# Performance work log

Measured on AMD Instinct MI355X. Metric: run time of the kernel, lower is better.

Reference implementation:

```python
import jax, jax.numpy as jnp
import numpy as np

B, N, D, H = 256, 64, 128, 64

def _w(key, shape, fan_in):
    return jax.random.normal(key, shape, jnp.float32) * (1.0 / np.sqrt(fan_in))

def setup_inputs() -> dict:
    key = jax.random.key(0)
    ks = jax.random.split(key, 6)
    return {
        "observations": jax.random.normal(ks[0], (B, N, D), jnp.float32),
        "enc_w": _w(ks[1], (D, H), D), "enc_b": jnp.zeros((H,), jnp.float32),
        "gate_w1": _w(ks[2], (2 * H, H), 2 * H), "gate_b1": jnp.zeros((H,), jnp.float32),
        "gate_w2": _w(ks[3], (H, 1), H), "gate_b2": jnp.zeros((1,), jnp.float32),
        "msg_w1": _w(ks[4], (H, H), H), "msg_b1": jnp.zeros((H,), jnp.float32),
        "msg_w2": _w(ks[5], (H, H), H), "msg_b2": jnp.zeros((H,), jnp.float32),
    }

def reference(observations, enc_w, enc_b, gate_w1, gate_b1, gate_w2, gate_b2,
              msg_w1, msg_b1, msg_w2, msg_b2):
    # encoder: (B, N, H)
    enc = jax.nn.relu(observations @ enc_w + enc_b)
    h = enc.shape[-1]
    # gate layer 1 on concat([e_i, e_j]) == e_i @ W_top + e_j @ W_bot; avoids
    # materializing the (B, N, N, 2H) concat tensor.
    w_i, w_j = gate_w1[:h], gate_w1[h:]
    gi = enc @ w_i                       # (B, N, H) contribution of receiver i
    gj = enc @ w_j + gate_b1             # (B, N, H) contribution of sender j
    hid = jax.nn.relu(gi[:, :, None, :] + gj[:, None, :, :])   # (B, N, N, H)
    gates = jax.nn.sigmoid(jnp.squeeze(hid @ gate_w2, -1) + gate_b2[0])  # (B, N, N)
    # message_gen(encoded): identical for every i in the original loop
    msg = jax.nn.relu(enc @ msg_w1 + msg_b1) @ msg_w2 + msg_b2  # (B, N, H)
    # enhanced[b, i] = sum_j gates[b, i, j] * msg[b, j]
    enhanced = jnp.einsum('bij,bjh->bih', gates, msg)           # (B, N, H)
    return enhanced
```

## Files before the change

### kernel.cpp

```cpp
#include <hip/hip_runtime.h>

typedef float  f32x4  __attribute__((ext_vector_type(4)));
typedef short  bf16x8 __attribute__((ext_vector_type(8)));

#define Bb 256

__device__ __forceinline__ uint cvtpk(float lo, float hi) {
    uint r;
    asm("v_cvt_pk_bf16_f32 %0, %1, %2" : "=v"(r) : "v"(lo), "v"(hi));
    return r;
}
__device__ __forceinline__ ushort f2b1(float v) { return (ushort)cvtpk(v, v); }
__device__ __forceinline__ float bflo(uint u) { return __uint_as_float(u << 16); }
__device__ __forceinline__ float bfhi(uint u) { return __uint_as_float(u & 0xffff0000u); }

union U8 { uint u[4]; bf16x8 v; };

__global__ __launch_bounds__(512, 4) void gcm_kernel(
    const float* __restrict__ obs,
    const float* __restrict__ enc_w,
    const float* __restrict__ enc_b,
    const float* __restrict__ gate_w1,
    const float* __restrict__ gate_b1,
    const float* __restrict__ gate_w2,
    const float* __restrict__ gate_b2,
    const float* __restrict__ msg_w1,
    const float* __restrict__ msg_b1,
    const float* __restrict__ msg_w2,
    const float* __restrict__ msg_b2,
    float* __restrict__ out)
{
    const int bid  = blockIdx.x;
    const int bb   = bid >> 1;
    const int half = bid & 1;
    const int t    = threadIdx.x;
    const int lane = t & 63;
    const int wv   = t >> 6;
    const int lr   = lane & 15;
    const int lg   = lane >> 4;
    const int rt   = wv >> 1;

    __shared__ __align__(16) char arena[74240];
    ushort* s_wT     = (ushort*)(arena);
    ushort* s_encwT  = (ushort*)(arena + 32768);
    float*  s_gi     = (float*) (arena + 32768);
    ushort* s_gatesb = (ushort*)(arena + 40960);
    ushort* s_enc    = (ushort*)(arena + 49152);
    ushort* s_msgT   = (ushort*)(arena + 49152);
    ushort* s_msgh   = (ushort*)(arena + 57344);
    ushort* s_gjb    = (ushort*)(arena + 65536);

    float4 pf[8];
    {
        const float* ob = obs + ((size_t)bb * 64 + rt * 16 + lr) * 128 + lg * 8;
        #pragma unroll
        for (int ks = 0; ks < 4; ++ks) {
            pf[2 * ks]     = *(const float4*)(ob + ks * 32);
            pf[2 * ks + 1] = *(const float4*)(ob + ks * 32 + 4);
        }
    }
    float4 pe[4];
    #pragma unroll
    for (int it = 0; it < 4; ++it) {
        const int idx = t + it * 512;
        const int k   = idx >> 4;
        const int n0  = (idx & 15) * 4;
        pe[it] = *(const float4*)(enc_w + k * 64 + n0);
    }
    bf16x8 afrag[4];
    #pragma unroll
    for (int ks = 0; ks < 4; ++ks) {
        U8 u;
        u.u[0] = cvtpk(pf[2 * ks].x,     pf[2 * ks].y);
        u.u[1] = cvtpk(pf[2 * ks].z,     pf[2 * ks].w);
        u.u[2] = cvtpk(pf[2 * ks + 1].x, pf[2 * ks + 1].y);
        u.u[3] = cvtpk(pf[2 * ks + 1].z, pf[2 * ks + 1].w);
        afrag[ks] = u.v;
    }
    #pragma unroll
    for (int it = 0; it < 4; ++it) {
        const int idx = t + it * 512;
        const int k   = idx >> 4;
        const int n0  = (idx & 15) * 4;
        uint pA = cvtpk(pe[it].x, pe[it].y), pB = cvtpk(pe[it].z, pe[it].w);
        s_encwT[((n0 + 0) * 128 + k) ^ (((n0 + 0) & 7) << 3)] = (ushort)pA;
        s_encwT[((n0 + 1) * 128 + k) ^ (((n0 + 1) & 7) << 3)] = (ushort)(pA >> 16);
        s_encwT[((n0 + 2) * 128 + k) ^ (((n0 + 2) & 7) << 3)] = (ushort)pB;
        s_encwT[((n0 + 3) * 128 + k) ^ (((n0 + 3) & 7) << 3)] = (ushort)(pB >> 16);
    }
    float4 pfw[8];
    {
        const int k  = t >> 4;
        const int n0 = (t & 15) * 4;
        #pragma unroll
        for (int kh = 0; kh < 2; ++kh) {
            const int kk = k + kh * 32;
            pfw[0 * 2 + kh] = *(const float4*)(gate_w1 + kk * 64 + n0);
            pfw[1 * 2 + kh] = *(const float4*)(gate_w1 + (64 + kk) * 64 + n0);
            pfw[2 * 2 + kh] = *(const float4*)(msg_w1 + kk * 64 + n0);
            pfw[3 * 2 + kh] = *(const float4*)(msg_w2 + kk * 64 + n0);
        }
    }
    __syncthreads();

    {
        f32x4 acc[2];
        acc[0] = (f32x4){0.f, 0.f, 0.f, 0.f};
        acc[1] = (f32x4){0.f, 0.f, 0.f, 0.f};
        #pragma unroll
        for (int ks = 0; ks < 4; ++ks) {
            const int k0 = ks * 32 + lg * 8;
            #pragma unroll
            for (int jj = 0; jj < 2; ++jj) {
                const int n = (wv & 1) * 32 + jj * 16 + lr;
                bf16x8 bf = *(const bf16x8*)(s_encwT + ((n * 128 + k0) ^ ((n & 7) << 3)));
                acc[jj] = __builtin_amdgcn_mfma_f32_16x16x32_bf16(afrag[ks], bf, acc[jj], 0, 0, 0);
            }
        }
        {
            const int k  = t >> 4;
            const int n00 = (t & 15) * 4;
            #pragma unroll
            for (int m = 0; m < 4; ++m) {
                #pragma unroll
                for (int kh = 0; kh < 2; ++kh) {
                    float4 w4 = pfw[m * 2 + kh];
                    const int kk = k + kh * 32;
                    const int nb = m * 64 + n00;
                    uint pA = cvtpk(w4.x, w4.y), pB = cvtpk(w4.z, w4.w);
                    s_wT[((nb + 0) * 64 + kk) ^ (((nb + 0) & 7) << 3)] = (ushort)pA;
                    s_wT[((nb + 1) * 64 + kk) ^ (((nb + 1) & 7) << 3)] = (ushort)(pA >> 16);
                    s_wT[((nb + 2) * 64 + kk) ^ (((nb + 2) & 7) << 3)] = (ushort)pB;
                    s_wT[((nb + 3) * 64 + kk) ^ (((nb + 3) & 7) << 3)] = (ushort)(pB >> 16);
                }
            }
        }
        const int rb = rt * 16 + lg * 4;
        #pragma unroll
        for (int jj = 0; jj < 2; ++jj) {
            const int n = (wv & 1) * 32 + jj * 16 + lr;
            const float be = enc_b[n];
            #pragma unroll
            for (int rr = 0; rr < 4; ++rr) {
                const int row = rb + rr;
                float v = fmaxf(acc[jj][rr] + be, 0.f);
                s_enc[(row * 64 + n) ^ ((row & 7) << 3)] = f2b1(v);
            }
        }
    }
    __syncthreads();

    {
        f32x4 acc[6];
        #pragma unroll
        for (int q = 0; q < 6; ++q) acc[q] = (f32x4){0.f, 0.f, 0.f, 0.f};
        const int arow = rt * 16 + lr;
        #pragma unroll
        for (int ks = 0; ks < 2; ++ks) {
            const int k0 = ks * 32 + lg * 8;
            bf16x8 a = *(const bf16x8*)(s_enc + ((arow * 64 + k0) ^ ((arow & 7) << 3)));
            #pragma unroll
            for (int q = 0; q < 6; ++q) {
                const int n = ((wv & 1) * 6 + q) * 16 + lr;
                bf16x8 bf = *(const bf16x8*)(s_wT + ((n * 64 + k0) ^ ((n & 7) << 3)));
                acc[q] = __builtin_amdgcn_mfma_f32_16x16x32_bf16(a, bf, acc[q], 0, 0, 0);
            }
        }
        const int rb = rt * 16 + lg * 4;
        #pragma unroll
        for (int q = 0; q < 6; ++q) {
            const int nfull = ((wv & 1) * 6 + q) * 16;
            const int cc = nfull + lr;
            if (nfull < 64) {
                if ((rt >> 1) == half) {
                    const int lb = rb - half * 32;
                    #pragma unroll
                    for (int rr = 0; rr < 4; ++rr) {
                        const int row = lb + rr;
                        s_gi[(row * 64 + cc) ^ ((row & 7) << 2)] = acc[q][rr];
                    }
                }
            } else if (nfull < 128) {
                const float b1 = gate_b1[cc - 64];
                #pragma unroll
                for (int rr = 0; rr < 4; ++rr)
                    s_gjb[(rb + rr) * 68 + (cc - 64)] = f2b1(acc[q][rr] + b1);
            } else {
                const float bm = msg_b1[cc - 128];
                float v0 = fmaxf(acc[q][0] + bm, 0.f), v1 = fmaxf(acc[q][1] + bm, 0.f);
                float v2 = fmaxf(acc[q][2] + bm, 0.f), v3 = fmaxf(acc[q][3] + bm, 0.f);
                uint pA = cvtpk(v0, v1), pB = cvtpk(v2, v3);
                const int c2 = cc - 128;
                s_msgh[((rb + 0) * 64 + c2) ^ (((rb + 0) & 7) << 3)] = (ushort)pA;
                s_msgh[((rb + 1) * 64 + c2) ^ (((rb + 1) & 7) << 3)] = (ushort)(pA >> 16);
                s_msgh[((rb + 2) * 64 + c2) ^ (((rb + 2) & 7) << 3)] = (ushort)pB;
                s_msgh[((rb + 3) * 64 + c2) ^ (((rb + 3) & 7) << 3)] = (ushort)(pB >> 16);
            }
        }
    }
    __syncthreads();

    {
        f32x4 acc[2];
        acc[0] = (f32x4){0.f, 0.f, 0.f, 0.f};
        acc[1] = (f32x4){0.f, 0.f, 0.f, 0.f};
        const int arow = rt * 16 + lr;
        #pragma unroll
        for (int ks = 0; ks < 2; ++ks) {
            const int k0 = ks * 32 + lg * 8;
            bf16x8 a = *(const bf16x8*)(s_msgh + ((arow * 64 + k0) ^ ((arow & 7) << 3)));
            #pragma unroll
            for (int jj = 0; jj < 2; ++jj) {
                const int n = 192 + ((wv & 1) * 2 + jj) * 16 + lr;
                bf16x8 bf = *(const bf16x8*)(s_wT + ((n * 64 + k0) ^ ((n & 7) << 3)));
                acc[jj] = __builtin_amdgcn_mfma_f32_16x16x32_bf16(a, bf, acc[jj], 0, 0, 0);
            }
        }
        const int jb = rt * 16 + lg * 4;
        #pragma unroll
        for (int jj = 0; jj < 2; ++jj) {
            const int h = ((wv & 1) * 2 + jj) * 16 + lr;
            const float bm2 = msg_b2[h];
            uint pA = cvtpk(acc[jj][0] + bm2, acc[jj][1] + bm2);
            uint pB = cvtpk(acc[jj][2] + bm2, acc[jj][3] + bm2);
            const int e = (h * 64 + jb) ^ ((h & 7) << 3);
            *(uint*)(s_msgT + e)     = pA;
            *(uint*)(s_msgT + e + 2) = pB;
        }
    }

    {
        const int lrow0 = wv * 4;
        float ag[4] = {0.f, 0.f, 0.f, 0.f};
        const ushort* gjrow = s_gjb + lane * 68;
        #pragma unroll
        for (int h0 = 0; h0 < 64; h0 += 8) {
            uint2 pj0 = *(const uint2*)(gjrow + h0);
            uint2 pj1 = *(const uint2*)(gjrow + h0 + 4);
            float gj0 = bflo(pj0.x), gj1 = bfhi(pj0.x), gj2 = bflo(pj0.y), gj3 = bfhi(pj0.y);
            float gj4 = bflo(pj1.x), gj5 = bfhi(pj1.x), gj6 = bflo(pj1.y), gj7 = bfhi(pj1.y);
            float4 w2a = *(const float4*)(gate_w2 + h0);
            float4 w2b = *(const float4*)(gate_w2 + h0 + 4);
            #pragma unroll
            for (int r = 0; r < 4; ++r) {
                const int row = lrow0 + r;
                float4 gia = *(const float4*)(s_gi + ((row * 64 + h0) ^ ((row & 7) << 2)));
                float4 gib = *(const float4*)(s_gi + ((row * 64 + h0 + 4) ^ ((row & 7) << 2)));
                ag[r] = fmaf(fmaxf(gia.x + gj0, 0.f), w2a.x, ag[r]);
                ag[r] = fmaf(fmaxf(gia.y + gj1, 0.f), w2a.y, ag[r]);
                ag[r] = fmaf(fmaxf(gia.z + gj2, 0.f), w2a.z, ag[r]);
                ag[r] = fmaf(fmaxf(gia.w + gj3, 0.f), w2a.w, ag[r]);
                ag[r] = fmaf(fmaxf(gib.x + gj4, 0.f), w2b.x, ag[r]);
                ag[r] = fmaf(fmaxf(gib.y + gj5, 0.f), w2b.y, ag[r]);
                ag[r] = fmaf(fmaxf(gib.z + gj6, 0.f), w2b.z, ag[r]);
                ag[r] = fmaf(fmaxf(gib.w + gj7, 0.f), w2b.w, ag[r]);
            }
        }
        const float b2v = gate_b2[0];
        #pragma unroll
        for (int r = 0; r < 4; ++r) {
            const int row = lrow0 + r;
            const float g = 1.f / (1.f + __expf(-(ag[r] + b2v)));
            s_gatesb[(row * 64 + lane) ^ ((row & 7) << 3)] = f2b1(g);
        }
    }
    __syncthreads();

    {
        const int rtl = wv >> 2;
        const int ct  = wv & 3;
        f32x4 acc = (f32x4){0.f, 0.f, 0.f, 0.f};
        const int arow = rtl * 16 + lr;
        const int n = ct * 16 + lr;
        #pragma unroll
        for (int ks = 0; ks < 2; ++ks) {
            const int k0 = ks * 32 + lg * 8;
            bf16x8 a  = *(const bf16x8*)(s_gatesb + ((arow * 64 + k0) ^ ((arow & 7) << 3)));
            bf16x8 bf = *(const bf16x8*)(s_msgT   + ((n * 64 + k0) ^ ((n & 7) << 3)));
            acc = __builtin_amdgcn_mfma_f32_16x16x32_bf16(a, bf, acc, 0, 0, 0);
        }
        const int rb = half * 32 + rtl * 16 + lg * 4;
        #pragma unroll
        for (int rr = 0; rr < 4; ++rr)
            out[((size_t)bb * 64 + rb + rr) * 64 + n] = acc[rr];
    }
}

extern "C" void kernel_launch(void* const* d_in, const int* in_sizes, int n_in,
                              void* d_out, int out_size, void* d_ws, size_t ws_size,
                              hipStream_t stream) {
    const float* obs     = (const float*)d_in[0];
    const float* enc_w   = (const float*)d_in[1];
    const float* enc_b   = (const float*)d_in[2];
    const float* gate_w1 = (const float*)d_in[3];
    const float* gate_b1 = (const float*)d_in[4];
    const float* gate_w2 = (const float*)d_in[5];
    const float* gate_b2 = (const float*)d_in[6];
    const float* msg_w1  = (const float*)d_in[7];
    const float* msg_b1  = (const float*)d_in[8];
    const float* msg_w2  = (const float*)d_in[9];
    const float* msg_b2  = (const float*)d_in[10];
    float* out = (float*)d_out;

    gcm_kernel<<<2 * Bb, 512, 0, stream>>>(obs, enc_w, enc_b, gate_w1, gate_b1,
                                           gate_w2, gate_b2, msg_w1, msg_b1,
                                           msg_w2, msg_b2, out);
}
```

Measured before the change: 22.33 us.

## Split fused kernel into projection and gating kernels via workspace buffers

Splits the single fused kernel into two launches. The first computes encoder, gate projections and messages for only half the rows per block, removing the duplicated per-batch work, and writes gi, gj and transposed messages in bf16 to a global workspace. The second kernel computes the pairwise gates and the final einsum from those buffers. A single-kernel fallback with 1024 threads per block runs when the workspace is too small. The split adds an extra launch, a global round trip for the intermediates, and bf16 rounding of gi.

```diff
diff --git a/kernel.cpp b/kernel.cpp
--- a/kernel.cpp
+++ b/kernel.cpp
@@ -16,43 +16,34 @@
 
 union U8 { uint u[4]; bf16x8 v; };
 
-__global__ __launch_bounds__(512, 4) void gcm_kernel(
-    const float* __restrict__ obs,
-    const float* __restrict__ enc_w,
-    const float* __restrict__ enc_b,
-    const float* __restrict__ gate_w1,
-    const float* __restrict__ gate_b1,
-    const float* __restrict__ gate_w2,
-    const float* __restrict__ gate_b2,
-    const float* __restrict__ msg_w1,
-    const float* __restrict__ msg_b1,
-    const float* __restrict__ msg_w2,
+__global__ __launch_bounds__(512, 4) void gcm_ka(
+    const float* __restrict__ obs, const float* __restrict__ enc_w,
+    const float* __restrict__ enc_b, const float* __restrict__ gate_w1,
+    const float* __restrict__ gate_b1, const float* __restrict__ msg_w1,
+    const float* __restrict__ msg_b1, const float* __restrict__ msg_w2,
     const float* __restrict__ msg_b2,
-    float* __restrict__ out)
+    ushort* __restrict__ gi_g, ushort* __restrict__ gj_g, ushort* __restrict__ msgT_g)
 {
-    const int bid  = blockIdx.x;
-    const int bb   = bid >> 1;
-    const int half = bid & 1;
+    const int bid = blockIdx.x;
+    const int bb  = bid >> 1;
+    const int hR  = bid & 1;
     const int t    = threadIdx.x;
     const int lane = t & 63;
     const int wv   = t >> 6;
     const int lr   = lane & 15;
     const int lg   = lane >> 4;
-    const int rt   = wv >> 1;
-
-    __shared__ __align__(16) char arena[74240];
-    ushort* s_wT     = (ushort*)(arena);
-    ushort* s_encwT  = (ushort*)(arena + 32768);
-    float*  s_gi     = (float*) (arena + 32768);
-    ushort* s_gatesb = (ushort*)(arena + 40960);
-    ushort* s_enc    = (ushort*)(arena + 49152);
-    ushort* s_msgT   = (ushort*)(arena + 49152);
-    ushort* s_msgh   = (ushort*)(arena + 57344);
-    ushort* s_gjb    = (ushort*)(arena + 65536);
+    const int rt   = wv >> 2;
+    const int ct   = wv & 3;
+
+    __shared__ __align__(16) char arena[57344];
+    ushort* s_wT    = (ushort*)(arena);
+    ushort* s_encwT = (ushort*)(arena + 32768);
+    ushort* s_enc   = (ushort*)(arena + 49152);
+    ushort* s_msgh  = (ushort*)(arena + 53248);
 
     float4 pf[8];
     {
-        const float* ob = obs + ((size_t)bb * 64 + rt * 16 + lr) * 128 + lg * 8;
+        const float* ob = obs + ((size_t)bb * 64 + hR * 32 + rt * 16 + lr) * 128 + lg * 8;
         #pragma unroll
         for (int ks = 0; ks < 4; ++ks) {
             pf[2 * ks]     = *(const float4*)(ob + ks * 32);
@@ -104,21 +95,16 @@
     __syncthreads();
 
     {
-        f32x4 acc[2];
-        acc[0] = (f32x4){0.f, 0.f, 0.f, 0.f};
-        acc[1] = (f32x4){0.f, 0.f, 0.f, 0.f};
+        f32x4 acc = (f32x4){0.f, 0.f, 0.f, 0.f};
+        const int n = ct * 16 + lr;
         #pragma unroll
         for (int ks = 0; ks < 4; ++ks) {
             const int k0 = ks * 32 + lg * 8;
-            #pragma unroll
-            for (int jj = 0; jj < 2; ++jj) {
-                const int n = (wv & 1) * 32 + jj * 16 + lr;
-                bf16x8 bf = *(const bf16x8*)(s_encwT + ((n * 128 + k0) ^ ((n & 7) << 3)));
-                acc[jj] = __builtin_amdgcn_mfma_f32_16x16x32_bf16(afrag[ks], bf, acc[jj], 0, 0, 0);
-            }
+            bf16x8 bf = *(const bf16x8*)(s_encwT + ((n * 128 + k0) ^ ((n & 7) << 3)));
+            acc = __builtin_amdgcn_mfma_f32_16x16x32_bf16(afrag[ks], bf, acc, 0, 0, 0);
         }
         {
-            const int k  = t >> 4;
+            const int k   = t >> 4;
             const int n00 = (t & 15) * 4;
             #pragma unroll
             for (int m = 0; m < 4; ++m) {
@@ -136,55 +122,46 @@
             }
         }
         const int rb = rt * 16 + lg * 4;
-        #pragma unroll
-        for (int jj = 0; jj < 2; ++jj) {
-            const int n = (wv & 1) * 32 + jj * 16 + lr;
-            const float be = enc_b[n];
-            #pragma unroll
-            for (int rr = 0; rr < 4; ++rr) {
-                const int row = rb + rr;
-                float v = fmaxf(acc[jj][rr] + be, 0.f);
-                s_enc[(row * 64 + n) ^ ((row & 7) << 3)] = f2b1(v);
-            }
-        }
-    }
-    __syncthreads();
-
-    {
-        f32x4 acc[6];
-        #pragma unroll
-        for (int q = 0; q < 6; ++q) acc[q] = (f32x4){0.f, 0.f, 0.f, 0.f};
+        const float be = enc_b[n];
+        #pragma unroll
+        for (int rr = 0; rr < 4; ++rr) {
+            const int row = rb + rr;
+            float v = fmaxf(acc[rr] + be, 0.f);
+            s_enc[(row * 64 + n) ^ ((row & 7) << 3)] = f2b1(v);
+        }
+    }
+    __syncthreads();
+
+    {
+        f32x4 acc[3];
+        #pragma unroll
+        for (int q = 0; q < 3; ++q) acc[q] = (f32x4){0.f, 0.f, 0.f, 0.f};
         const int arow = rt * 16 + lr;
         #pragma unroll
         for (int ks = 0; ks < 2; ++ks) {
             const int k0 = ks * 32 + lg * 8;
             bf16x8 a = *(const bf16x8*)(s_enc + ((arow * 64 + k0) ^ ((arow & 7) << 3)));
             #pragma unroll
-            for (int q = 0; q < 6; ++q) {
-                const int n = ((wv & 1) * 6 + q) * 16 + lr;
+            for (int q = 0; q < 3; ++q) {
+                const int n = (ct * 3 + q) * 16 + lr;
                 bf16x8 bf = *(const bf16x8*)(s_wT + ((n * 64 + k0) ^ ((n & 7) << 3)));
                 acc[q] = __builtin_amdgcn_mfma_f32_16x16x32_bf16(a, bf, acc[q], 0, 0, 0);
             }
         }
         const int rb = rt * 16 + lg * 4;
         #pragma unroll
-        for (int q = 0; q < 6; ++q) {
-            const int nfull = ((wv & 1) * 6 + q) * 16;
+        for (int q = 0; q < 3; ++q) {
+            const int nfull = (ct * 3 + q) * 16;
             const int cc = nfull + lr;
             if (nfull < 64) {
-                if ((rt >> 1) == half) {
-                    const int lb = rb - half * 32;
-                    #pragma unroll
-                    for (int rr = 0; rr < 4; ++rr) {
-                        const int row = lb + rr;
-                        s_gi[(row * 64 + cc) ^ ((row & 7) << 2)] = acc[q][rr];
-                    }
-                }
+                #pragma unroll
+                for (int rr = 0; rr < 4; ++rr)
+                    gi_g[((size_t)bb * 64 + hR * 32 + rb + rr) * 64 + cc] = f2b1(acc[q][rr]);
             } else if (nfull < 128) {
                 const float b1 = gate_b1[cc - 64];
                 #pragma unroll
                 for (int rr = 0; rr < 4; ++rr)
-                    s_gjb[(rb + rr) * 68 + (cc - 64)] = f2b1(acc[q][rr] + b1);
+                    gj_g[((size_t)bb * 64 + hR * 32 + rb + rr) * 64 + (cc - 64)] = f2b1(acc[q][rr] + b1);
             } else {
                 const float bm = msg_b1[cc - 128];
                 float v0 = fmaxf(acc[q][0] + bm, 0.f), v1 = fmaxf(acc[q][1] + bm, 0.f);
@@ -201,77 +178,87 @@
     __syncthreads();
 
     {
-        f32x4 acc[2];
-        acc[0] = (f32x4){0.f, 0.f, 0.f, 0.f};
-        acc[1] = (f32x4){0.f, 0.f, 0.f, 0.f};
+        f32x4 acc = (f32x4){0.f, 0.f, 0.f, 0.f};
         const int arow = rt * 16 + lr;
+        const int n = 192 + ct * 16 + lr;
         #pragma unroll
         for (int ks = 0; ks < 2; ++ks) {
             const int k0 = ks * 32 + lg * 8;
-            bf16x8 a = *(const bf16x8*)(s_msgh + ((arow * 64 + k0) ^ ((arow & 7) << 3)));
-            #pragma unroll
-            for (int jj = 0; jj < 2; ++jj) {
-                const int n = 192 + ((wv & 1) * 2 + jj) * 16 + lr;
-                bf16x8 bf = *(const bf16x8*)(s_wT + ((n * 64 + k0) ^ ((n & 7) << 3)));
-                acc[jj] = __builtin_amdgcn_mfma_f32_16x16x32_bf16(a, bf, acc[jj], 0, 0, 0);
-            }
-        }
-        const int jb = rt * 16 + lg * 4;
-        #pragma unroll
-        for (int jj = 0; jj < 2; ++jj) {
-            const int h = ((wv & 1) * 2 + jj) * 16 + lr;
-            const float bm2 = msg_b2[h];
-            uint pA = cvtpk(acc[jj][0] + bm2, acc[jj][1] + bm2);
-            uint pB = cvtpk(acc[jj][2] + bm2, acc[jj][3] + bm2);
-            const int e = (h * 64 + jb) ^ ((h & 7) << 3);
-            *(uint*)(s_msgT + e)     = pA;
-            *(uint*)(s_msgT + e + 2) = pB;
-        }
-    }
-
-    {
-        const int lrow0 = wv * 4;
-        float ag[4] = {0.f, 0.f, 0.f, 0.f};
-        const ushort* gjrow = s_gjb + lane * 68;
-        #pragma unroll
-        for (int h0 = 0; h0 < 64; h0 += 8) {
-            uint2 pj0 = *(const uint2*)(gjrow + h0);
-            uint2 pj1 = *(const uint2*)(gjrow + h0 + 4);
-            float gj0 = bflo(pj0.x), gj1 = bfhi(pj0.x), gj2 = bflo(pj0.y), gj3 = bfhi(pj0.y);
-            float gj4 = bflo(pj1.x), gj5 = bfhi(pj1.x), gj6 = bflo(pj1.y), gj7 = bfhi(pj1.y);
-            float4 w2a = *(const float4*)(gate_w2 + h0);
-            float4 w2b = *(const float4*)(gate_w2 + h0 + 4);
-            #pragma unroll
-            for (int r = 0; r < 4; ++r) {
-                const int row = lrow0 + r;
-                float4 gia = *(const float4*)(s_gi + ((row * 64 + h0) ^ ((row & 7) << 2)));
-                float4 gib = *(const float4*)(s_gi + ((row * 64 + h0 + 4) ^ ((row & 7) << 2)));
-                ag[r] = fmaf(fmaxf(gia.x + gj0, 0.f), w2a.x, ag[r]);
-                ag[r] = fmaf(fmaxf(gia.y + gj1, 0.f), w2a.y, ag[r]);
-                ag[r] = fmaf(fmaxf(gia.z + gj2, 0.f), w2a.z, ag[r]);
-                ag[r] = fmaf(fmaxf(gia.w + gj3, 0.f), w2a.w, ag[r]);
-                ag[r] = fmaf(fmaxf(gib.x + gj4, 0.f), w2b.x, ag[r]);
-                ag[r] = fmaf(fmaxf(gib.y + gj5, 0.f), w2b.y, ag[r]);
-                ag[r] = fmaf(fmaxf(gib.z + gj6, 0.f), w2b.z, ag[r]);
-                ag[r] = fmaf(fmaxf(gib.w + gj7, 0.f), w2b.w, ag[r]);
-            }
-        }
-        const float b2v = gate_b2[0];
-        #pragma unroll
-        for (int r = 0; r < 4; ++r) {
-            const int row = lrow0 + r;
-            const float g = 1.f / (1.f + __expf(-(ag[r] + b2v)));
-            s_gatesb[(row * 64 + lane) ^ ((row & 7) << 3)] = f2b1(g);
-        }
-    }
-    __syncthreads();
-
-    {
-        const int rtl = wv >> 2;
-        const int ct  = wv & 3;
+            bf16x8 a  = *(const bf16x8*)(s_msgh + ((arow * 64 + k0) ^ ((arow & 7) << 3)));
+            bf16x8 bf = *(const bf16x8*)(s_wT + ((n * 64 + k0) ^ ((n & 7) << 3)));
+            acc = __builtin_amdgcn_mfma_f32_16x16x32_bf16(a, bf, acc, 0, 0, 0);
+        }
+        const int h  = ct * 16 + lr;
+        const int jg = hR * 32 + rt * 16 + lg * 4;
+        const float bm2 = msg_b2[h];
+        uint pA = cvtpk(acc[0] + bm2, acc[1] + bm2);
+        uint pB = cvtpk(acc[2] + bm2, acc[3] + bm2);
+        uint* dst = (uint*)(msgT_g + ((size_t)bb * 64 + h) * 64 + jg);
+        dst[0] = pA;
+        dst[1] = pB;
+    }
+}
+
+__global__ __launch_bounds__(512, 4) void gcm_kb(
+    const float* __restrict__ gate_w2, const float* __restrict__ gate_b2,
+    const ushort* __restrict__ gi_g, const ushort* __restrict__ gj_g,
+    const ushort* __restrict__ msgT_g, float* __restrict__ out)
+{
+    const int bid = blockIdx.x;
+    const int bb  = bid >> 1;
+    const int hR  = bid & 1;
+    const int t    = threadIdx.x;
+    const int lane = t & 63;
+    const int wv   = t >> 6;
+    const int lr   = lane & 15;
+    const int lg   = lane >> 4;
+
+    __shared__ __align__(16) ushort s_msgT[64 * 64];
+    __shared__ __align__(16) ushort s_gatesb[32 * 64];
+
+    {
+        const int h = t >> 3, q = t & 7;
+        uint4 v = *(const uint4*)(msgT_g + ((size_t)bb * 64 + h) * 64 + q * 8);
+        *(uint4*)(s_msgT + ((h * 64 + q * 8) ^ ((h & 7) << 3))) = v;
+    }
+
+    float gjv[64];
+    {
+        const ushort* gp = gj_g + ((size_t)bb * 64 + lane) * 64;
+        #pragma unroll
+        for (int c = 0; c < 8; ++c) {
+            uint4 p = *(const uint4*)(gp + c * 8);
+            gjv[c * 8 + 0] = bflo(p.x); gjv[c * 8 + 1] = bfhi(p.x);
+            gjv[c * 8 + 2] = bflo(p.y); gjv[c * 8 + 3] = bfhi(p.y);
+            gjv[c * 8 + 4] = bflo(p.z); gjv[c * 8 + 5] = bfhi(p.z);
+            gjv[c * 8 + 6] = bflo(p.w); gjv[c * 8 + 7] = bfhi(p.w);
+        }
+    }
+    const float b2v = gate_b2[0];
+
+    #pragma unroll
+    for (int r = 0; r < 4; ++r) {
+        const int lrow = wv * 4 + r;
+        const int grow = __builtin_amdgcn_readfirstlane(hR * 32 + lrow);
+        const uint* gip = (const uint*)(gi_g + ((size_t)bb * 64 + grow) * 64);
+        float acc = 0.f;
+        #pragma unroll
+        for (int c = 0; c < 32; ++c) {
+            const uint p = gip[c];
+            const float g0 = bflo(p), g1 = bfhi(p);
+            acc = fmaf(fmaxf(g0 + gjv[2 * c],     0.f), gate_w2[2 * c],     acc);
+            acc = fmaf(fmaxf(g1 + gjv[2 * c + 1], 0.f), gate_w2[2 * c + 1], acc);
+        }
+        const float g = 1.f / (1.f + __expf(-(acc + b2v)));
+        s_gatesb[(lrow * 64 + lane) ^ ((lrow & 7) << 3)] = f2b1(g);
+    }
+    __syncthreads();
+
+    {
+        const int rtl = wv >> 2, ctl = wv & 3;
         f32x4 acc = (f32x4){0.f, 0.f, 0.f, 0.f};
         const int arow = rtl * 16 + lr;
-        const int n = ct * 16 + lr;
+        const int n = ctl * 16 + lr;
         #pragma unroll
         for (int ks = 0; ks < 2; ++ks) {
             const int k0 = ks * 32 + lg * 8;
@@ -279,7 +266,220 @@
             bf16x8 bf = *(const bf16x8*)(s_msgT   + ((n * 64 + k0) ^ ((n & 7) << 3)));
             acc = __builtin_amdgcn_mfma_f32_16x16x32_bf16(a, bf, acc, 0, 0, 0);
         }
-        const int rb = half * 32 + rtl * 16 + lg * 4;
+        const int rb = hR * 32 + rtl * 16 + lg * 4;
+        #pragma unroll
+        for (int rr = 0; rr < 4; ++rr)
+            out[((size_t)bb * 64 + rb + rr) * 64 + n] = acc[rr];
+    }
+}
+
+__global__ __launch_bounds__(1024) void gcm_fb(
+    const float* __restrict__ obs, const float* __restrict__ enc_w,
+    const float* __restrict__ enc_b, const float* __restrict__ gate_w1,
+    const float* __restrict__ gate_b1, const float* __restrict__ gate_w2,
+    const float* __restrict__ gate_b2, const float* __restrict__ msg_w1,
+    const float* __restrict__ msg_b1, const float* __restrict__ msg_w2,
+    const float* __restrict__ msg_b2, float* __restrict__ out)
+{
+    const int bb   = blockIdx.x;
+    const int t    = threadIdx.x;
+    const int lane = t & 63;
+    const int wv   = t >> 6;
+    const int lr   = lane & 15;
+    const int lg   = lane >> 4;
+    const int rt   = wv & 3;
+    const int ct   = wv >> 2;
+
+    __shared__ __align__(16) ushort s_encwT[64 * 128];
+    __shared__ __align__(16) ushort s_wT[256 * 64];
+    __shared__ __align__(16) ushort s_enc[64 * 64];
+    __shared__ __align__(16) ushort s_msgh[64 * 64];
+    __shared__ __align__(16) ushort s_gatesb[64 * 64];
+    __shared__ __align__(16) ushort s_msgT[64 * 64];
+    __shared__ __align__(16) float  s_gi[64 * 64];
+    __shared__ __align__(16) float  s_gj[64 * 64];
+    __shared__ __align__(16) float  s_w2[64];
+
+    float4 pf[8];
+    {
+        const float* ob = obs + ((size_t)bb * 64 + rt * 16 + lr) * 128 + lg * 8;
+        #pragma unroll
+        for (int ks = 0; ks < 4; ++ks) {
+            pf[2 * ks]     = *(const float4*)(ob + ks * 32);
+            pf[2 * ks + 1] = *(const float4*)(ob + ks * 32 + 4);
+        }
+    }
+    if (t < 64) s_w2[t] = gate_w2[t];
+    #pragma unroll
+    for (int it = 0; it < 2; ++it) {
+        const int g  = t + it * 1024;
+        const int k  = g >> 4;
+        const int n0 = (g & 15) * 4;
+        float4 w4 = *(const float4*)(enc_w + k * 64 + n0);
+        uint pA = cvtpk(w4.x, w4.y), pB = cvtpk(w4.z, w4.w);
+        s_encwT[((n0 + 0) * 128 + k) ^ (((n0 + 0) & 7) << 3)] = (ushort)pA;
+        s_encwT[((n0 + 1) * 128 + k) ^ (((n0 + 1) & 7) << 3)] = (ushort)(pA >> 16);
+        s_encwT[((n0 + 2) * 128 + k) ^ (((n0 + 2) & 7) << 3)] = (ushort)pB;
+        s_encwT[((n0 + 3) * 128 + k) ^ (((n0 + 3) & 7) << 3)] = (ushort)(pB >> 16);
+    }
+    bf16x8 afrag[4];
+    #pragma unroll
+    for (int ks = 0; ks < 4; ++ks) {
+        U8 u;
+        u.u[0] = cvtpk(pf[2 * ks].x,     pf[2 * ks].y);
+        u.u[1] = cvtpk(pf[2 * ks].z,     pf[2 * ks].w);
+        u.u[2] = cvtpk(pf[2 * ks + 1].x, pf[2 * ks + 1].y);
+        u.u[3] = cvtpk(pf[2 * ks + 1].z, pf[2 * ks + 1].w);
+        afrag[ks] = u.v;
+    }
+    float4 pfw[4];
+    {
+        const int k  = t >> 4;
+        const int n0 = (t & 15) * 4;
+        pfw[0] = *(const float4*)(gate_w1 + k * 64 + n0);
+        pfw[1] = *(const float4*)(gate_w1 + (64 + k) * 64 + n0);
+        pfw[2] = *(const float4*)(msg_w1 + k * 64 + n0);
+        pfw[3] = *(const float4*)(msg_w2 + k * 64 + n0);
+    }
+    __syncthreads();
+    {
+        f32x4 acc = (f32x4){0.f, 0.f, 0.f, 0.f};
+        const int n = ct * 16 + lr;
+        #pragma unroll
+        for (int ks = 0; ks < 4; ++ks) {
+            const int k0 = ks * 32 + lg * 8;
+            bf16x8 bf = *(const bf16x8*)(s_encwT + ((n * 128 + k0) ^ ((n & 7) << 3)));
+            acc = __builtin_amdgcn_mfma_f32_16x16x32_bf16(afrag[ks], bf, acc, 0, 0, 0);
+        }
+        #pragma unroll
+        for (int it = 0; it < 4; ++it) {
+            const int k  = t >> 4;
+            const int n0 = it * 64 + (t & 15) * 4;
+            uint pA = cvtpk(pfw[it].x, pfw[it].y), pB = cvtpk(pfw[it].z, pfw[it].w);
+            s_wT[((n0 + 0) * 64 + k) ^ (((n0 + 0) & 7) << 3)] = (ushort)pA;
+            s_wT[((n0 + 1) * 64 + k) ^ (((n0 + 1) & 7) << 3)] = (ushort)(pA >> 16);
+            s_wT[((n0 + 2) * 64 + k) ^ (((n0 + 2) & 7) << 3)] = (ushort)pB;
+            s_wT[((n0 + 3) * 64 + k) ^ (((n0 + 3) & 7) << 3)] = (ushort)(pB >> 16);
+        }
+        const float be = enc_b[n];
+        float v0 = fmaxf(acc[0] + be, 0.f), v1 = fmaxf(acc[1] + be, 0.f);
+        float v2 = fmaxf(acc[2] + be, 0.f), v3 = fmaxf(acc[3] + be, 0.f);
+        uint pA = cvtpk(v0, v1), pB = cvtpk(v2, v3);
+        const int rb = rt * 16 + lg * 4;
+        s_enc[((rb + 0) * 64 + n) ^ (((rb + 0) & 7) << 3)] = (ushort)pA;
+        s_enc[((rb + 1) * 64 + n) ^ (((rb + 1) & 7) << 3)] = (ushort)(pA >> 16);
+        s_enc[((rb + 2) * 64 + n) ^ (((rb + 2) & 7) << 3)] = (ushort)pB;
+        s_enc[((rb + 3) * 64 + n) ^ (((rb + 3) & 7) << 3)] = (ushort)(pB >> 16);
+    }
+    __syncthreads();
+    {
+        f32x4 acc[3];
+        #pragma unroll
+        for (int q = 0; q < 3; ++q) acc[q] = (f32x4){0.f, 0.f, 0.f, 0.f};
+        const int arow = rt * 16 + lr;
+        #pragma unroll
+        for (int ks = 0; ks < 2; ++ks) {
+            const int k0 = ks * 32 + lg * 8;
+            bf16x8 a = *(const bf16x8*)(s_enc + ((arow * 64 + k0) ^ ((arow & 7) << 3)));
+            #pragma unroll
+            for (int q = 0; q < 3; ++q) {
+                const int n = (ct * 3 + q) * 16 + lr;
+                bf16x8 bf = *(const bf16x8*)(s_wT + ((n * 64 + k0) ^ ((n & 7) << 3)));
+                acc[q] = __builtin_amdgcn_mfma_f32_16x16x32_bf16(a, bf, acc[q], 0, 0, 0);
+            }
+        }
+        const int rb = rt * 16 + lg * 4;
+        #pragma unroll
+        for (int q = 0; q < 3; ++q) {
+            const int nfull = (ct * 3 + q) * 16;
+            const int cc = nfull + lr;
+            if (nfull < 64) {
+                #pragma unroll
+                for (int rr = 0; rr < 4; ++rr) {
+                    const int row = rb + rr;
+                    s_gi[(row * 64 + cc) ^ ((row & 7) << 2)] = acc[q][rr];
+                }
+            } else if (nfull < 128) {
+                const float b1 = gate_b1[cc - 64];
+                #pragma unroll
+                for (int rr = 0; rr < 4; ++rr) {
+                    const int row = rb + rr;
+                    s_gj[(row * 64 + (cc - 64)) ^ ((row & 7) << 2)] = acc[q][rr] + b1;
+                }
+            } else {
+                const float bm = msg_b1[cc - 128];
+                float v0 = fmaxf(acc[q][0] + bm, 0.f), v1 = fmaxf(acc[q][1] + bm, 0.f);
+                float v2 = fmaxf(acc[q][2] + bm, 0.f), v3 = fmaxf(acc[q][3] + bm, 0.f);
+                uint pA = cvtpk(v0, v1), pB = cvtpk(v2, v3);
+                const int c2 = cc - 128;
+                s_msgh[((rb + 0) * 64 + c2) ^ (((rb + 0) & 7) << 3)] = (ushort)pA;
+                s_msgh[((rb + 1) * 64 + c2) ^ (((rb + 1) & 7) << 3)] = (ushort)(pA >> 16);
+                s_msgh[((rb + 2) * 64 + c2) ^ (((rb + 2) & 7) << 3)] = (ushort)pB;
+                s_msgh[((rb + 3) * 64 + c2) ^ (((rb + 3) & 7) << 3)] = (ushort)(pB >> 16);
+            }
+        }
+    }
+    __syncthreads();
+    {
+        f32x4 acc = (f32x4){0.f, 0.f, 0.f, 0.f};
+        const int arow = rt * 16 + lr;
+        const int nn3 = 192 + ct * 16 + lr;
+        #pragma unroll
+        for (int ks = 0; ks < 2; ++ks) {
+            const int k0 = ks * 32 + lg * 8;
+            bf16x8 a = *(const bf16x8*)(s_msgh + ((arow * 64 + k0) ^ ((arow & 7) << 3)));
+            bf16x8 bf = *(const bf16x8*)(s_wT + ((nn3 * 64 + k0) ^ ((nn3 & 7) << 3)));
+            acc = __builtin_amdgcn_mfma_f32_16x16x32_bf16(a, bf, acc, 0, 0, 0);
+        }
+        const int h  = ct * 16 + lr;
+        const int jb = rt * 16 + lg * 4;
+        const float bm2 = msg_b2[h];
+        uint pA = cvtpk(acc[0] + bm2, acc[1] + bm2);
+        uint pB = cvtpk(acc[2] + bm2, acc[3] + bm2);
+        const int e = (h * 64 + jb) ^ ((h & 7) << 3);
+        *(uint*)(s_msgT + e)     = pA;
+        *(uint*)(s_msgT + e + 2) = pB;
+    }
+    {
+        const int row0g = wv * 4;
+        float ag[4] = {0.f, 0.f, 0.f, 0.f};
+        #pragma unroll 4
+        for (int h0 = 0; h0 < 64; h0 += 4) {
+            float4 gj4 = *(const float4*)&s_gj[(lane * 64 + h0) ^ ((lane & 7) << 2)];
+            float4 w24 = *(const float4*)&s_w2[h0];
+            #pragma unroll
+            for (int r = 0; r < 4; ++r) {
+                const int row = row0g + r;
+                float4 gi4 = *(const float4*)&s_gi[(row * 64 + h0) ^ ((row & 7) << 2)];
+                ag[r] = fmaf(fmaxf(gi4.x + gj4.x, 0.f), w24.x, ag[r]);
+                ag[r] = fmaf(fmaxf(gi4.y + gj4.y, 0.f), w24.y, ag[r]);
+                ag[r] = fmaf(fmaxf(gi4.z + gj4.z, 0.f), w24.z, ag[r]);
+                ag[r] = fmaf(fmaxf(gi4.w + gj4.w, 0.f), w24.w, ag[r]);
+            }
+        }
+        const float b2v = gate_b2[0];
+        #pragma unroll
+        for (int r = 0; r < 4; ++r) {
+            const int row = row0g + r;
+            const float g = 1.f / (1.f + __expf(-(ag[r] + b2v)));
+            s_gatesb[(row * 64 + lane) ^ ((row & 7) << 3)] = f2b1(g);
+        }
+    }
+    __syncthreads();
+    {
+        const int rtl = wv >> 2;
+        const int ctl = wv & 3;
+        f32x4 acc = (f32x4){0.f, 0.f, 0.f, 0.f};
+        const int arow = rtl * 16 + lr;
+        const int n = ctl * 16 + lr;
+        #pragma unroll
+        for (int ks = 0; ks < 2; ++ks) {
+            const int k0 = ks * 32 + lg * 8;
+            bf16x8 a  = *(const bf16x8*)(s_gatesb + ((arow * 64 + k0) ^ ((arow & 7) << 3)));
+            bf16x8 bf = *(const bf16x8*)(s_msgT   + ((n * 64 + k0) ^ ((n & 7) << 3)));
+            acc = __builtin_amdgcn_mfma_f32_16x16x32_bf16(a, bf, acc, 0, 0, 0);
+        }
+        const int rb = rtl * 16 + lg * 4;
         #pragma unroll
         for (int rr = 0; rr < 4; ++rr)
             out[((size_t)bb * 64 + rb + rr) * 64 + n] = acc[rr];
@@ -302,7 +502,19 @@
     const float* msg_b2  = (const float*)d_in[10];
     float* out = (float*)d_out;
 
-    gcm_kernel<<<2 * Bb, 512, 0, stream>>>(obs, enc_w, enc_b, gate_w1, gate_b1,
-                                           gate_w2, gate_b2, msg_w1, msg_b1,
-                                           msg_w2, msg_b2, out);
+    const size_t per = (size_t)Bb * 64 * 64;
+    const size_t need = 3 * per * sizeof(ushort);
+    if (ws_size >= need) {
+        ushort* gi_g   = (ushort*)d_ws;
+        ushort* gj_g   = gi_g + per;
+        ushort* msgT_g = gj_g + per;
+        gcm_ka<<<2 * Bb, 512, 0, stream>>>(obs, enc_w, enc_b, gate_w1, gate_b1,
+                                           msg_w1, msg_b1, msg_w2, msg_b2,
+                                           gi_g, gj_g, msgT_g);
+        gcm_kb<<<2 * Bb, 512, 0, stream>>>(gate_w2, gate_b2, gi_g, gj_g, msgT_g, out);
+    } else {
+        gcm_fb<<<Bb, 1024, 0, stream>>>(obs, enc_w, enc_b, gate_w1, gate_b1,
+                                        gate_w2, gate_b2, msg_w1, msg_b1,
+                                        msg_w2, msg_b2, out);
+    }
 }
```

Result: slower. 27.49 us (+23.1%).
